# Kernel optimization log

Hardware: AMD Instinct MI355X
Metric: run time of the kernel (lower is better)

## Reference

```python
import jax, jax.numpy as jnp
import numpy as np

B, T, C, H = 8, 2048, 1024, 128  # batch, seq, n_embed, head_size


def setup_inputs() -> dict:
    key = jax.random.key(0)
    ks = jax.random.split(key, 7)
    s = 1.0 / np.sqrt(C)
    return {
        "x": jax.random.normal(ks[0], (B, T, C), dtype=jnp.float32),
        "Wq": jax.random.uniform(ks[1], (C, H), jnp.float32, -s, s),
        "bq": jax.random.uniform(ks[2], (H,), jnp.float32, -s, s),
        "Wk": jax.random.uniform(ks[3], (C, H), jnp.float32, -s, s),
        "bk": jax.random.uniform(ks[4], (H,), jnp.float32, -s, s),
        "Wv": jax.random.uniform(ks[5], (C, H), jnp.float32, -s, s),
        "bv": jax.random.uniform(ks[6], (H,), jnp.float32, -s, s),
    }


def reference(x, Wq, bq, Wk, bk, Wv, bv):
    # Projections: [B, T, H]
    Q = jnp.einsum("btc,ch->bth", x, Wq) + bq
    K = jnp.einsum("btc,ch->bth", x, Wk) + bk
    V = jnp.einsum("btc,ch->bth", x, Wv) + bv
    # Scores scaled by n_embed**-0.5 (faithful to source, which uses C not head_size)
    scale = jnp.asarray(C, x.dtype) ** -0.5
    scores = jnp.einsum("bqh,bkh->bqk", Q, K) * scale  # [B, T, T]
    causal = jnp.tril(jnp.ones((T, T), dtype=bool))
    scores = jnp.where(causal, scores, jnp.asarray(-jnp.inf, x.dtype))
    attn = jax.nn.softmax(scores, axis=-1)
    # dropout p=0.0 (eval) -> identity
    return jnp.einsum("bqk,bkh->bqh", attn, V)
```

## Files before the change

kernel.cpp:

```cpp
#include <hip/hip_runtime.h>
#include <hip/hip_bf16.h>
#include <math.h>

typedef __attribute__((ext_vector_type(4))) float f32x4;
typedef __attribute__((ext_vector_type(8))) short s16x8;
typedef __attribute__((ext_vector_type(4))) short s16x4;

#define NB 8
#define NT 2048
#define NC 1024
#define NH 128
#define QSCALE 0.04508422002778f
#define PIECES 80

__device__ __forceinline__ short f2bf(float f) {
  union { float f; unsigned u; } v; v.f = f;
  unsigned r = v.u + 0x7fffu + ((v.u >> 16) & 1u);
  return (short)(r >> 16);
}

__device__ __forceinline__ void glds16(const short* g, short* l) {
  __builtin_amdgcn_global_load_lds(
      (const __attribute__((address_space(1))) unsigned int*)g,
      (__attribute__((address_space(3))) unsigned int*)l, 16, 0, 0);
}

__global__ __launch_bounds__(256)
void wt_kernel(const float* __restrict__ Wq, const float* __restrict__ Wk,
               const float* __restrict__ Wv, short* __restrict__ Wt) {
  __shared__ short T[64 * 72];
  const int tid = threadIdx.x;
  const int k0 = blockIdx.x * 64, n0 = blockIdx.y * 64, proj = blockIdx.z;
  const float* W = (proj == 0) ? Wq : ((proj == 1) ? Wk : Wv);
#pragma unroll
  for (int u = 0; u < 4; u++) {
    int row = u * 16 + (tid >> 4);
    int col4 = (tid & 15) * 4;
    float4 v = *(const float4*)(W + (size_t)(k0 + row) * NH + n0 + col4);
    T[(col4 + 0) * 72 + row] = f2bf(v.x);
    T[(col4 + 1) * 72 + row] = f2bf(v.y);
    T[(col4 + 2) * 72 + row] = f2bf(v.z);
    T[(col4 + 3) * 72 + row] = f2bf(v.w);
  }
  __syncthreads();
#pragma unroll
  for (int u = 0; u < 2; u++) {
    int c = tid + 256 * u;
    int n = c >> 3, c8 = c & 7;
    s16x8 v = *(const s16x8*)(T + n * 72 + c8 * 8);
    *(s16x8*)(Wt + (size_t)proj * (NH * NC) + (size_t)(n0 + n) * NC + k0 + c8 * 8) = v;
  }
}

__global__ __launch_bounds__(256)
void proj_kernel(const float* __restrict__ x, const short* __restrict__ Wt,
                 const float* __restrict__ bq, const float* __restrict__ bk,
                 const float* __restrict__ bv,
                 short* __restrict__ Qb, short* __restrict__ Kb, short* __restrict__ Vtb) {
  __shared__ __align__(16) short smem[17408];
  short* As = smem;
  short* Bs = smem + 8192;

  const int tid = threadIdx.x;
  const int w = tid >> 6, lane = tid & 63;
  const int lr = lane & 15, lg = lane >> 4;
  const int proj = blockIdx.x;
  const int m0 = blockIdx.y * 128;
  const int msub = (w & 1) * 64, nsub = (w >> 1) * 64;

  const short* Wtp = Wt + (size_t)proj * (NH * NC);
  const float* asrc = x + (size_t)(m0 + (tid >> 1)) * NC + (tid & 1) * 32;
  const int arow = tid >> 1;

  f32x4 acc[4][4];
#pragma unroll
  for (int i = 0; i < 4; i++)
#pragma unroll
    for (int j = 0; j < 4; j++) acc[i][j] = {0.f, 0.f, 0.f, 0.f};

  float4 pa[8], pb_[8];
#pragma unroll
  for (int u = 0; u < 8; u++) pa[u] = *(const float4*)(asrc + u * 4);

  auto body = [&](int s, float4 (&cur)[8], float4 (&nxt)[8]) {
    const int k0 = s * 64;
    if (s < 15) {
#pragma unroll
      for (int u = 0; u < 8; u++) nxt[u] = *(const float4*)(asrc + k0 + 64 + u * 4);
    }
#pragma unroll
    for (int u = 0; u < 4; u++) {
      float4 a = cur[2 * u], b2 = cur[2 * u + 1];
      s16x8 v;
      v[0] = f2bf(a.x); v[1] = f2bf(a.y); v[2] = f2bf(a.z); v[3] = f2bf(a.w);
      v[4] = f2bf(b2.x); v[5] = f2bf(b2.y); v[6] = f2bf(b2.z); v[7] = f2bf(b2.w);
      int cc = (tid & 1) * 4 + u;
      *(s16x8*)(As + arow * 64 + ((cc ^ (arow & 7)) * 8)) = v;
    }
#pragma unroll
    for (int u = 0; u < 4; u++) {
      int boff = w * 4096 + u * 1024 + lane * 16;
      int n = boff >> 7, cc = (boff >> 4) & 7;
      glds16(Wtp + (size_t)n * NC + k0 + ((cc ^ (n & 7)) * 8), Bs + w * 2048 + u * 512);
    }
    __syncthreads();
#pragma unroll
    for (int kc = 0; kc < 2; kc++) {
      s16x8 af[4], bf[4];
#pragma unroll
      for (int mi = 0; mi < 4; mi++) {
        int row = msub + mi * 16 + lr;
        af[mi] = *(const s16x8*)(As + row * 64 + (((kc * 4 + lg) ^ (lr & 7)) * 8));
      }
#pragma unroll
      for (int ni = 0; ni < 4; ni++) {
        int row = nsub + ni * 16 + lr;
        bf[ni] = *(const s16x8*)(Bs + row * 64 + (((kc * 4 + lg) ^ (lr & 7)) * 8));
      }
#pragma unroll
      for (int mi = 0; mi < 4; mi++)
#pragma unroll
        for (int ni = 0; ni < 4; ni++)
          acc[mi][ni] = __builtin_amdgcn_mfma_f32_16x16x32_bf16(af[mi], bf[ni], acc[mi][ni], 0, 0, 0);
    }
    __syncthreads();
  };

  for (int ss = 0; ss < 8; ss++) { body(2 * ss, pa, pb_); body(2 * ss + 1, pb_, pa); }

  const float* bias = (proj == 0) ? bq : ((proj == 1) ? bk : bv);
  const float scl = (proj == 0) ? QSCALE : 1.0f;
  short* Tr = smem;

  if (proj < 2) {
#pragma unroll
    for (int mi = 0; mi < 4; mi++)
#pragma unroll
      for (int ni = 0; ni < 4; ni++) {
        float bn = bias[nsub + ni * 16 + lr];
        int d = nsub + ni * 16 + lr;
#pragma unroll
        for (int r = 0; r < 4; r++) {
          int t = msub + mi * 16 + lg * 4 + r;
          Tr[t * 136 + d] = f2bf((acc[mi][ni][r] + bn) * scl);
        }
      }
    __syncthreads();
    short* dst = (proj == 0) ? Qb : Kb;
#pragma unroll
    for (int i = 0; i < 8; i++) {
      int c = tid + 256 * i;
      int t = c >> 4, cc = c & 15;
      s16x8 v = *(const s16x8*)(Tr + t * 136 + cc * 8);
      *(s16x8*)(dst + (size_t)(m0 + t) * NH + cc * 8) = v;
    }
  } else {
#pragma unroll
    for (int mi = 0; mi < 4; mi++)
#pragma unroll
      for (int ni = 0; ni < 4; ni++) {
        float bn = bias[nsub + ni * 16 + lr];
        int d = nsub + ni * 16 + lr;
        int t0 = msub + mi * 16 + lg * 4;
        s16x4 v;
        v[0] = f2bf(acc[mi][ni][0] + bn);
        v[1] = f2bf(acc[mi][ni][1] + bn);
        v[2] = f2bf(acc[mi][ni][2] + bn);
        v[3] = f2bf(acc[mi][ni][3] + bn);
        *(s16x4*)(Tr + d * 136 + t0) = v;
      }
    __syncthreads();
    int b = m0 >> 11, t0g = m0 & 2047;
#pragma unroll
    for (int i = 0; i < 8; i++) {
      int c = tid + 256 * i;
      int d = c >> 4, cc = c & 15;
      s16x8 v = *(const s16x8*)(Tr + d * 136 + cc * 8);
      *(s16x8*)(Vtb + (size_t)b * (NH * NT) + (size_t)d * NT + t0g + cc * 8) = v;
    }
  }
}

__global__ __launch_bounds__(256)
void attn_partial(const short* __restrict__ Qb, const short* __restrict__ Kb,
                  const short* __restrict__ Vtb, float* __restrict__ out,
                  float* __restrict__ part, float* __restrict__ partml) {
  __shared__ __align__(16) short smem[16384];

  const int tid = threadIdx.x;
  const int w = tid >> 6, lane = tid & 63;
  const int lr = lane & 15, lg = lane >> 4;

  const int batch = blockIdx.x;
  const int r = (PIECES - 1) - blockIdx.y;
  int j = 0, pfx = 0;
  while (pfx + (j >> 3) + 1 <= r) { pfx += (j >> 3) + 1; j++; }
  const int c = r - pfx;
  const int P = (j >> 3) + 1;
  const int q0 = j * 64;
  const int kv_begin = c * 512;
  const int kv_end = min(kv_begin + 512, (j + 1) * 64);
  const int nsteps = (kv_end - kv_begin) >> 5;

  const short* Kp = Kb + (size_t)batch * NT * NH;
  const short* Vp = Vtb + (size_t)batch * NH * NT;
  const int q = q0 + w * 16 + lr;

  const short* Qrow = Qb + (size_t)(batch * NT + q) * NH;
  s16x8 qf[4];
#pragma unroll
  for (int dc = 0; dc < 4; dc++) qf[dc] = *(const s16x8*)(Qrow + dc * 32 + lg * 8);

  f32x4 acc[8];
#pragma unroll
  for (int i = 0; i < 8; i++) acc[i] = {0.f, 0.f, 0.f, 0.f};
  float m_run = -3.0e38f, l_run = 0.f;

  auto stage = [&](int buf, int kv0) {
#pragma unroll
    for (int u = 0; u < 2; u++) {
      int boff = w * 2048 + u * 1024 + lane * 16;
      int row = boff >> 8, ch = (boff >> 4) & 15;
      int sch = (ch & 8) | ((ch & 7) ^ (row & 7));
      glds16(Kp + (size_t)(kv0 + row) * NH + sch * 8, smem + buf * 4096 + w * 1024 + u * 512);
    }
#pragma unroll
    for (int u = 0; u < 2; u++) {
      int boff = w * 2048 + u * 1024 + lane * 16;
      int d = boff >> 6, ch = (boff >> 4) & 3;
      int sch = ch ^ (d & 3);
      glds16(Vp + (size_t)d * NT + kv0 + sch * 8, smem + 8192 + buf * 4096 + w * 1024 + u * 512);
    }
  };

  stage(0, kv_begin);
  __syncthreads();

  for (int s = 0; s < nsteps; s++) {
    const int buf = s & 1;
    const int kv0 = kv_begin + s * 32;
    if (s + 1 < nsteps) stage(buf ^ 1, kv0 + 32);

    const short* Kl = smem + buf * 4096;
    const short* Vl = smem + 8192 + buf * 4096;

    f32x4 st0 = {0.f, 0.f, 0.f, 0.f}, st1 = st0;
#pragma unroll
    for (int dc = 0; dc < 4; dc++) {
      int ch = dc * 4 + lg;
      int sch = (ch & 8) | ((ch & 7) ^ (lr & 7));
      s16x8 k0f = *(const s16x8*)(Kl + lr * 128 + sch * 8);
      s16x8 k1f = *(const s16x8*)(Kl + (16 + lr) * 128 + sch * 8);
      st0 = __builtin_amdgcn_mfma_f32_16x16x32_bf16(k0f, qf[dc], st0, 0, 0, 0);
      st1 = __builtin_amdgcn_mfma_f32_16x16x32_bf16(k1f, qf[dc], st1, 0, 0, 0);
    }
    if (kv0 + 31 > q0) {
#pragma unroll
      for (int rr = 0; rr < 4; rr++) {
        if (kv0 + lg * 4 + rr > q) st0[rr] = -3.0e38f;
        if (kv0 + 16 + lg * 4 + rr > q) st1[rr] = -3.0e38f;
      }
    }
    float tm = -3.0e38f;
#pragma unroll
    for (int rr = 0; rr < 4; rr++) { tm = fmaxf(tm, st0[rr]); tm = fmaxf(tm, st1[rr]); }
    tm = fmaxf(tm, __shfl_xor(tm, 16, 64));
    tm = fmaxf(tm, __shfl_xor(tm, 32, 64));
    float m_new = fmaxf(m_run, tm);
    float corr = exp2f(m_run - m_new);
    float psum = 0.f;
    s16x8 pf;
#pragma unroll
    for (int rr = 0; rr < 4; rr++) {
      float p0 = exp2f(st0[rr] - m_new);
      float p1 = exp2f(st1[rr] - m_new);
      psum += p0 + p1;
      pf[rr] = f2bf(p0);
      pf[4 + rr] = f2bf(p1);
    }
    psum += __shfl_xor(psum, 16, 64);
    psum += __shfl_xor(psum, 32, 64);
    l_run = l_run * corr + psum;
    m_run = m_new;
#pragma unroll
    for (int i = 0; i < 8; i++) acc[i] *= corr;
#pragma unroll
    for (int dm = 0; dm < 8; dm++) {
      int d = dm * 16 + lr;
      const short* vb = Vl + d * 32;
      int c0 = (lg >> 1) ^ (d & 3);
      int c1 = c0 ^ 2;
      s16x4 v0 = *(const s16x4*)(vb + c0 * 8 + (lg & 1) * 4);
      s16x4 v1 = *(const s16x4*)(vb + c1 * 8 + (lg & 1) * 4);
      s16x8 vf = __builtin_shufflevector(v0, v1, 0, 1, 2, 3, 4, 5, 6, 7);
      acc[dm] = __builtin_amdgcn_mfma_f32_16x16x32_bf16(vf, pf, acc[dm], 0, 0, 0);
    }
    __syncthreads();
  }

  if (P == 1) {
    const float inv = 1.f / l_run;
    float* orow = out + (size_t)(batch * NT + q) * NH;
#pragma unroll
    for (int dm = 0; dm < 8; dm++) {
      f32x4 v = acc[dm] * inv;
      *(f32x4*)(orow + dm * 16 + lg * 4) = v;
    }
  } else {
    float* pb = part + ((size_t)batch * PIECES + r) * 8192;
    int ql = w * 16 + lr;
#pragma unroll
    for (int dm = 0; dm < 8; dm++)
      *(f32x4*)(pb + ql * 128 + dm * 16 + lg * 4) = acc[dm];
    if (lg == 0) {
      float2* ml = (float2*)partml + ((size_t)batch * PIECES + r) * 64;
      ml[ql] = make_float2(m_run, l_run);
    }
  }
}

__global__ __launch_bounds__(256)
void attn_combine(const float* __restrict__ part, const float* __restrict__ partml,
                  float* __restrict__ out) {
  const int batch = blockIdx.x;
  const int j = 8 + blockIdx.y;
  int pfx = 0;
  for (int jj = 0; jj < j; jj++) pfx += (jj >> 3) + 1;
  const int P = (j >> 3) + 1;
  const int tid = threadIdx.x;
  const int ql = tid >> 2, d0 = (tid & 3) * 32;

  const float2* mlb = (const float2*)partml + ((size_t)batch * PIECES + pfx) * 64 + ql;
  float M = -3.0e38f;
  for (int p = 0; p < P; p++) M = fmaxf(M, mlb[p * 64].x);
  float L = 0.f;
  f32x4 o[8];
#pragma unroll
  for (int u = 0; u < 8; u++) o[u] = {0.f, 0.f, 0.f, 0.f};
  for (int p = 0; p < P; p++) {
    float2 ml = mlb[p * 64];
    float wgt = exp2f(ml.x - M);
    L += wgt * ml.y;
    const float* pb = part + ((size_t)batch * PIECES + pfx + p) * 8192 + ql * 128 + d0;
#pragma unroll
    for (int u = 0; u < 8; u++) o[u] += wgt * *(const f32x4*)(pb + u * 4);
  }
  const float inv = 1.f / L;
  float* orow = out + ((size_t)batch * NT + j * 64 + ql) * NH + d0;
#pragma unroll
  for (int u = 0; u < 8; u++) *(f32x4*)(orow + u * 4) = o[u] * inv;
}

extern "C" void kernel_launch(void* const* d_in, const int* in_sizes, int n_in,
                              void* d_out, int out_size, void* d_ws, size_t ws_size,
                              hipStream_t stream) {
  const float* x = (const float*)d_in[0];
  const float* Wq = (const float*)d_in[1];
  const float* bq = (const float*)d_in[2];
  const float* Wk = (const float*)d_in[3];
  const float* bk = (const float*)d_in[4];
  const float* Wv = (const float*)d_in[5];
  const float* bv = (const float*)d_in[6];
  float* out = (float*)d_out;

  char* ws = (char*)d_ws;
  short* Wt = (short*)ws;
  short* Qb = (short*)(ws + 786432);
  short* Kb = (short*)(ws + 786432 + 4194304);
  short* Vtb = (short*)(ws + 786432 + 2 * 4194304);
  float* part = (float*)(ws + 13369344);
  float* partml = (float*)(ws + 13369344 + 20971520);

  wt_kernel<<<dim3(16, 2, 3), dim3(256), 0, stream>>>(Wq, Wk, Wv, Wt);
  proj_kernel<<<dim3(3, 128), dim3(256), 0, stream>>>(x, Wt, bq, bk, bv, Qb, Kb, Vtb);
  attn_partial<<<dim3(8, PIECES), dim3(256), 0, stream>>>(Qb, Kb, Vtb, out, part, partml);
  attn_combine<<<dim3(8, 24), dim3(256), 0, stream>>>(part, partml, out);
}
```

Baseline: 206.6 us.

## Retile projection GEMM with double buffering and widen attention KV step to 64

The projection kernel now uses 64-row M tiles (twice as many blocks), double-buffered LDS for A and B, and occupancy hints. The attention kernel now processes 64 keys per step instead of 32, with larger double-buffered K/V tiles and an adjusted V swizzle, which halves the number of barriers and softmax rescales. The bf16 conversion is switched to the library intrinsic. These changes raise LDS use and register pressure per block, which may limit occupancy in exchange for fewer sync steps and better overlap.

Result: faster. 177.1 us (-14.3%).

```diff
diff --git a/kernel.cpp b/kernel.cpp
--- a/kernel.cpp
+++ b/kernel.cpp
@@ -14,9 +14,9 @@
 #define PIECES 80
 
 __device__ __forceinline__ short f2bf(float f) {
-  union { float f; unsigned u; } v; v.f = f;
-  unsigned r = v.u + 0x7fffu + ((v.u >> 16) & 1u);
-  return (short)(r >> 16);
+  __hip_bfloat16 h = __float2bfloat16(f);
+  union { __hip_bfloat16 h; short s; } u; u.h = h;
+  return u.s;
 }
 
 __device__ __forceinline__ void glds16(const short* g, short* l) {
@@ -52,81 +52,95 @@
   }
 }
 
-__global__ __launch_bounds__(256)
+__global__ __launch_bounds__(256, 3)
 void proj_kernel(const float* __restrict__ x, const short* __restrict__ Wt,
                  const float* __restrict__ bq, const float* __restrict__ bk,
                  const float* __restrict__ bv,
                  short* __restrict__ Qb, short* __restrict__ Kb, short* __restrict__ Vtb) {
-  __shared__ __align__(16) short smem[17408];
-  short* As = smem;
-  short* Bs = smem + 8192;
+  __shared__ __align__(16) short smem[2 * 12288];
 
   const int tid = threadIdx.x;
   const int w = tid >> 6, lane = tid & 63;
   const int lr = lane & 15, lg = lane >> 4;
   const int proj = blockIdx.x;
-  const int m0 = blockIdx.y * 128;
-  const int msub = (w & 1) * 64, nsub = (w >> 1) * 64;
+  const int m0 = blockIdx.y * 64;
+  const int msub = (w & 1) * 32, nsub = (w >> 1) * 64;
 
   const short* Wtp = Wt + (size_t)proj * (NH * NC);
-  const float* asrc = x + (size_t)(m0 + (tid >> 1)) * NC + (tid & 1) * 32;
-  const int arow = tid >> 1;
-
-  f32x4 acc[4][4];
-#pragma unroll
-  for (int i = 0; i < 4; i++)
+  const int arow = tid >> 2, aq = tid & 3;
+  const float* asrc = x + (size_t)(m0 + arow) * NC + aq * 16;
+
+  f32x4 acc[2][4];
+#pragma unroll
+  for (int i = 0; i < 2; i++)
 #pragma unroll
     for (int j = 0; j < 4; j++) acc[i][j] = {0.f, 0.f, 0.f, 0.f};
 
-  float4 pa[8], pb_[8];
-#pragma unroll
-  for (int u = 0; u < 8; u++) pa[u] = *(const float4*)(asrc + u * 4);
-
-  auto body = [&](int s, float4 (&cur)[8], float4 (&nxt)[8]) {
-    const int k0 = s * 64;
-    if (s < 15) {
-#pragma unroll
-      for (int u = 0; u < 8; u++) nxt[u] = *(const float4*)(asrc + k0 + 64 + u * 4);
-    }
-#pragma unroll
-    for (int u = 0; u < 4; u++) {
-      float4 a = cur[2 * u], b2 = cur[2 * u + 1];
+  float4 pa[2][4];
+
+  auto loadA = [&](int slot, int k0) {
+#pragma unroll
+    for (int u = 0; u < 4; u++) pa[slot][u] = *(const float4*)(asrc + k0 + u * 4);
+  };
+  auto writeA = [&](int slot, int buf) {
+    short* As = smem + buf * 12288;
+#pragma unroll
+    for (int h = 0; h < 2; h++) {
+      float4 a = pa[slot][2 * h], b2 = pa[slot][2 * h + 1];
       s16x8 v;
       v[0] = f2bf(a.x); v[1] = f2bf(a.y); v[2] = f2bf(a.z); v[3] = f2bf(a.w);
       v[4] = f2bf(b2.x); v[5] = f2bf(b2.y); v[6] = f2bf(b2.z); v[7] = f2bf(b2.w);
-      int cc = (tid & 1) * 4 + u;
+      int cc = aq * 2 + h;
       *(s16x8*)(As + arow * 64 + ((cc ^ (arow & 7)) * 8)) = v;
     }
+  };
+  auto stageB = [&](int buf, int k0) {
+    short* Bs = smem + buf * 12288 + 4096;
 #pragma unroll
     for (int u = 0; u < 4; u++) {
-      int boff = w * 4096 + u * 1024 + lane * 16;
-      int n = boff >> 7, cc = (boff >> 4) & 7;
-      glds16(Wtp + (size_t)n * NC + k0 + ((cc ^ (n & 7)) * 8), Bs + w * 2048 + u * 512);
-    }
-    __syncthreads();
+      int c = u * 256 + w * 64 + lane;
+      int n = c >> 3, ch = c & 7;
+      glds16(Wtp + (size_t)n * NC + k0 + ((ch ^ (n & 7)) * 8),
+             Bs + (u * 256 + w * 64) * 8);
+    }
+  };
+  auto compute = [&](int buf) {
+    const short* As = smem + buf * 12288;
+    const short* Bs = smem + buf * 12288 + 4096;
 #pragma unroll
     for (int kc = 0; kc < 2; kc++) {
-      s16x8 af[4], bf[4];
-#pragma unroll
-      for (int mi = 0; mi < 4; mi++) {
+      s16x8 af[2], bf[4];
+#pragma unroll
+      for (int mi = 0; mi < 2; mi++) {
         int row = msub + mi * 16 + lr;
-        af[mi] = *(const s16x8*)(As + row * 64 + (((kc * 4 + lg) ^ (lr & 7)) * 8));
+        af[mi] = *(const s16x8*)(As + row * 64 + (((kc * 4 + lg) ^ (row & 7)) * 8));
       }
 #pragma unroll
       for (int ni = 0; ni < 4; ni++) {
         int row = nsub + ni * 16 + lr;
-        bf[ni] = *(const s16x8*)(Bs + row * 64 + (((kc * 4 + lg) ^ (lr & 7)) * 8));
-      }
-#pragma unroll
-      for (int mi = 0; mi < 4; mi++)
+        bf[ni] = *(const s16x8*)(Bs + row * 64 + (((kc * 4 + lg) ^ (row & 7)) * 8));
+      }
+#pragma unroll
+      for (int mi = 0; mi < 2; mi++)
 #pragma unroll
         for (int ni = 0; ni < 4; ni++)
           acc[mi][ni] = __builtin_amdgcn_mfma_f32_16x16x32_bf16(af[mi], bf[ni], acc[mi][ni], 0, 0, 0);
     }
+  };
+
+  loadA(0, 0);
+  stageB(0, 0);
+  writeA(0, 0);
+  __syncthreads();
+
+  for (int s = 0; s < 16; ++s) {
+    int buf = s & 1;
+    int slot = (s + 1) & 1;
+    if (s < 15) { loadA(slot, (s + 1) * 64); stageB(buf ^ 1, (s + 1) * 64); }
+    compute(buf);
+    if (s < 15) writeA(slot, buf ^ 1);
     __syncthreads();
-  };
-
-  for (int ss = 0; ss < 8; ss++) { body(2 * ss, pa, pb_); body(2 * ss + 1, pb_, pa); }
+  }
 
   const float* bias = (proj == 0) ? bq : ((proj == 1) ? bk : bv);
   const float scl = (proj == 0) ? QSCALE : 1.0f;
@@ -134,11 +148,11 @@
 
   if (proj < 2) {
 #pragma unroll
-    for (int mi = 0; mi < 4; mi++)
+    for (int mi = 0; mi < 2; mi++)
 #pragma unroll
       for (int ni = 0; ni < 4; ni++) {
-        float bn = bias[nsub + ni * 16 + lr];
         int d = nsub + ni * 16 + lr;
+        float bn = bias[d];
 #pragma unroll
         for (int r = 0; r < 4; r++) {
           int t = msub + mi * 16 + lg * 4 + r;
@@ -148,7 +162,7 @@
     __syncthreads();
     short* dst = (proj == 0) ? Qb : Kb;
 #pragma unroll
-    for (int i = 0; i < 8; i++) {
+    for (int i = 0; i < 4; i++) {
       int c = tid + 256 * i;
       int t = c >> 4, cc = c & 15;
       s16x8 v = *(const s16x8*)(Tr + t * 136 + cc * 8);
@@ -156,36 +170,36 @@
     }
   } else {
 #pragma unroll
-    for (int mi = 0; mi < 4; mi++)
+    for (int mi = 0; mi < 2; mi++)
 #pragma unroll
       for (int ni = 0; ni < 4; ni++) {
-        float bn = bias[nsub + ni * 16 + lr];
         int d = nsub + ni * 16 + lr;
+        float bn = bias[d];
         int t0 = msub + mi * 16 + lg * 4;
         s16x4 v;
         v[0] = f2bf(acc[mi][ni][0] + bn);
         v[1] = f2bf(acc[mi][ni][1] + bn);
         v[2] = f2bf(acc[mi][ni][2] + bn);
         v[3] = f2bf(acc[mi][ni][3] + bn);
-        *(s16x4*)(Tr + d * 136 + t0) = v;
+        *(s16x4*)(Tr + d * 72 + t0) = v;
       }
     __syncthreads();
     int b = m0 >> 11, t0g = m0 & 2047;
 #pragma unroll
-    for (int i = 0; i < 8; i++) {
+    for (int i = 0; i < 4; i++) {
       int c = tid + 256 * i;
-      int d = c >> 4, cc = c & 15;
-      s16x8 v = *(const s16x8*)(Tr + d * 136 + cc * 8);
+      int d = c >> 3, cc = c & 7;
+      s16x8 v = *(const s16x8*)(Tr + d * 72 + cc * 8);
       *(s16x8*)(Vtb + (size_t)b * (NH * NT) + (size_t)d * NT + t0g + cc * 8) = v;
     }
   }
 }
 
-__global__ __launch_bounds__(256)
+__global__ __launch_bounds__(256, 2)
 void attn_partial(const short* __restrict__ Qb, const short* __restrict__ Kb,
                   const short* __restrict__ Vtb, float* __restrict__ out,
                   float* __restrict__ part, float* __restrict__ partml) {
-  __shared__ __align__(16) short smem[16384];
+  __shared__ __align__(16) short smem[32768];
 
   const int tid = threadIdx.x;
   const int w = tid >> 6, lane = tid & 63;
@@ -200,7 +214,7 @@
   const int q0 = j * 64;
   const int kv_begin = c * 512;
   const int kv_end = min(kv_begin + 512, (j + 1) * 64);
-  const int nsteps = (kv_end - kv_begin) >> 5;
+  const int nsteps = (kv_end - kv_begin) >> 6;
 
   const short* Kp = Kb + (size_t)batch * NT * NH;
   const short* Vp = Vtb + (size_t)batch * NH * NT;
@@ -218,18 +232,20 @@
 
   auto stage = [&](int buf, int kv0) {
 #pragma unroll
-    for (int u = 0; u < 2; u++) {
-      int boff = w * 2048 + u * 1024 + lane * 16;
-      int row = boff >> 8, ch = (boff >> 4) & 15;
+    for (int u = 0; u < 4; u++) {
+      int c2 = u * 256 + w * 64 + lane;
+      int row = c2 >> 4, ch = c2 & 15;
       int sch = (ch & 8) | ((ch & 7) ^ (row & 7));
-      glds16(Kp + (size_t)(kv0 + row) * NH + sch * 8, smem + buf * 4096 + w * 1024 + u * 512);
-    }
-#pragma unroll
-    for (int u = 0; u < 2; u++) {
-      int boff = w * 2048 + u * 1024 + lane * 16;
-      int d = boff >> 6, ch = (boff >> 4) & 3;
-      int sch = ch ^ (d & 3);
-      glds16(Vp + (size_t)d * NT + kv0 + sch * 8, smem + 8192 + buf * 4096 + w * 1024 + u * 512);
+      glds16(Kp + (size_t)(kv0 + row) * NH + sch * 8,
+             smem + buf * 8192 + (u * 256 + w * 64) * 8);
+    }
+#pragma unroll
+    for (int u = 0; u < 4; u++) {
+      int c2 = u * 256 + w * 64 + lane;
+      int d = c2 >> 3, ch = c2 & 7;
+      int sch = ch ^ (d & 7);
+      glds16(Vp + (size_t)d * NT + kv0 + sch * 8,
+             smem + 16384 + buf * 8192 + (u * 256 + w * 64) * 8);
     }
   };
 
@@ -238,46 +254,51 @@
 
   for (int s = 0; s < nsteps; s++) {
     const int buf = s & 1;
-    const int kv0 = kv_begin + s * 32;
-    if (s + 1 < nsteps) stage(buf ^ 1, kv0 + 32);
-
-    const short* Kl = smem + buf * 4096;
-    const short* Vl = smem + 8192 + buf * 4096;
-
-    f32x4 st0 = {0.f, 0.f, 0.f, 0.f}, st1 = st0;
+    const int kv0 = kv_begin + s * 64;
+    if (s + 1 < nsteps) stage(buf ^ 1, kv0 + 64);
+
+    const short* Kl = smem + buf * 8192;
+    const short* Vl = smem + 16384 + buf * 8192;
+
+    f32x4 st[4];
+#pragma unroll
+    for (int sub = 0; sub < 4; sub++) st[sub] = {0.f, 0.f, 0.f, 0.f};
 #pragma unroll
     for (int dc = 0; dc < 4; dc++) {
       int ch = dc * 4 + lg;
       int sch = (ch & 8) | ((ch & 7) ^ (lr & 7));
-      s16x8 k0f = *(const s16x8*)(Kl + lr * 128 + sch * 8);
-      s16x8 k1f = *(const s16x8*)(Kl + (16 + lr) * 128 + sch * 8);
-      st0 = __builtin_amdgcn_mfma_f32_16x16x32_bf16(k0f, qf[dc], st0, 0, 0, 0);
-      st1 = __builtin_amdgcn_mfma_f32_16x16x32_bf16(k1f, qf[dc], st1, 0, 0, 0);
-    }
-    if (kv0 + 31 > q0) {
-#pragma unroll
-      for (int rr = 0; rr < 4; rr++) {
-        if (kv0 + lg * 4 + rr > q) st0[rr] = -3.0e38f;
-        if (kv0 + 16 + lg * 4 + rr > q) st1[rr] = -3.0e38f;
-      }
+#pragma unroll
+      for (int sub = 0; sub < 4; sub++) {
+        s16x8 kf = *(const s16x8*)(Kl + (sub * 16 + lr) * 128 + sch * 8);
+        st[sub] = __builtin_amdgcn_mfma_f32_16x16x32_bf16(kf, qf[dc], st[sub], 0, 0, 0);
+      }
+    }
+    if (kv0 + 63 > q0) {
+#pragma unroll
+      for (int sub = 0; sub < 4; sub++)
+#pragma unroll
+        for (int rr = 0; rr < 4; rr++)
+          if (kv0 + sub * 16 + lg * 4 + rr > q) st[sub][rr] = -3.0e38f;
     }
     float tm = -3.0e38f;
 #pragma unroll
-    for (int rr = 0; rr < 4; rr++) { tm = fmaxf(tm, st0[rr]); tm = fmaxf(tm, st1[rr]); }
+    for (int sub = 0; sub < 4; sub++)
+#pragma unroll
+      for (int rr = 0; rr < 4; rr++) tm = fmaxf(tm, st[sub][rr]);
     tm = fmaxf(tm, __shfl_xor(tm, 16, 64));
     tm = fmaxf(tm, __shfl_xor(tm, 32, 64));
     float m_new = fmaxf(m_run, tm);
     float corr = exp2f(m_run - m_new);
     float psum = 0.f;
-    s16x8 pf;
-#pragma unroll
-    for (int rr = 0; rr < 4; rr++) {
-      float p0 = exp2f(st0[rr] - m_new);
-      float p1 = exp2f(st1[rr] - m_new);
-      psum += p0 + p1;
-      pf[rr] = f2bf(p0);
-      pf[4 + rr] = f2bf(p1);
-    }
+    s16x8 pf[2];
+#pragma unroll
+    for (int sub = 0; sub < 4; sub++)
+#pragma unroll
+      for (int rr = 0; rr < 4; rr++) {
+        float p = exp2f(st[sub][rr] - m_new);
+        psum += p;
+        pf[sub >> 1][(sub & 1) * 4 + rr] = f2bf(p);
+      }
     psum += __shfl_xor(psum, 16, 64);
     psum += __shfl_xor(psum, 32, 64);
     l_run = l_run * corr + psum;
@@ -285,16 +306,18 @@
 #pragma unroll
     for (int i = 0; i < 8; i++) acc[i] *= corr;
 #pragma unroll
-    for (int dm = 0; dm < 8; dm++) {
-      int d = dm * 16 + lr;
-      const short* vb = Vl + d * 32;
-      int c0 = (lg >> 1) ^ (d & 3);
-      int c1 = c0 ^ 2;
-      s16x4 v0 = *(const s16x4*)(vb + c0 * 8 + (lg & 1) * 4);
-      s16x4 v1 = *(const s16x4*)(vb + c1 * 8 + (lg & 1) * 4);
-      s16x8 vf = __builtin_shufflevector(v0, v1, 0, 1, 2, 3, 4, 5, 6, 7);
-      acc[dm] = __builtin_amdgcn_mfma_f32_16x16x32_bf16(vf, pf, acc[dm], 0, 0, 0);
-    }
+    for (int ks = 0; ks < 2; ks++)
+#pragma unroll
+      for (int dm = 0; dm < 8; dm++) {
+        int d = dm * 16 + lr;
+        const short* vb = Vl + d * 64;
+        int ch0 = (ks * 4 + (lg >> 1)) ^ (d & 7);
+        int ch1 = ch0 ^ 2;
+        s16x4 v0 = *(const s16x4*)(vb + ch0 * 8 + (lg & 1) * 4);
+        s16x4 v1 = *(const s16x4*)(vb + ch1 * 8 + (lg & 1) * 4);
+        s16x8 vf = __builtin_shufflevector(v0, v1, 0, 1, 2, 3, 4, 5, 6, 7);
+        acc[dm] = __builtin_amdgcn_mfma_f32_16x16x32_bf16(vf, pf[ks], acc[dm], 0, 0, 0);
+      }
     __syncthreads();
   }
 
@@ -372,7 +395,7 @@
   float* partml = (float*)(ws + 13369344 + 20971520);
 
   wt_kernel<<<dim3(16, 2, 3), dim3(256), 0, stream>>>(Wq, Wk, Wv, Wt);
-  proj_kernel<<<dim3(3, 128), dim3(256), 0, stream>>>(x, Wt, bq, bk, bv, Qb, Kb, Vtb);
+  proj_kernel<<<dim3(3, 256), dim3(256), 0, stream>>>(x, Wt, bq, bk, bv, Qb, Kb, Vtb);
   attn_partial<<<dim3(8, PIECES), dim3(256), 0, stream>>>(Qb, Kb, Vtb, out, part, partml);
   attn_combine<<<dim3(8, 24), dim3(256), 0, stream>>>(part, partml, out);
 }
```
